# Optimization experiments

Hardware: AMD Instinct MI355X
Metric: run time of the kernel (lower is better)

## Reference

```python
import jax, jax.numpy as jnp
import numpy as np
from jax import lax

B, C, HID, H, W = 8, 256, 64, 64, 64

def conv3x3(x, w, b):
    # x: [B,C_in,H,W], w: [C_out,C_in,3,3], b: [C_out]
    y = lax.conv_general_dilated(x, w, window_strides=(1, 1), padding='SAME',
                                 dimension_numbers=('NCHW', 'OIHW', 'NCHW'))
    return y + b[None, :, None, None]

def setup_inputs() -> dict:
    key = jax.random.key(0)
    ks = jax.random.split(key, 7)
    s_in = 1.0 / np.sqrt(C * 9)
    return {
        'x': jax.random.normal(ks[0], (B, C, H, W), dtype=jnp.float32),
        'Wq': jax.random.normal(ks[1], (HID, C, 3, 3), dtype=jnp.float32) * s_in,
        'bq': jax.random.normal(ks[2], (HID,), dtype=jnp.float32) * s_in,
        'Wk': jax.random.normal(ks[3], (HID, C, 3, 3), dtype=jnp.float32) * s_in,
        'bk': jax.random.normal(ks[4], (HID,), dtype=jnp.float32) * s_in,
        'Wv': jax.random.normal(ks[5], (C, C, 3, 3), dtype=jnp.float32) * s_in,
        'bv': jax.random.normal(ks[6], (C,), dtype=jnp.float32) * s_in,
    }

def reference(x, Wq, bq, Wk, bk, Wv, bv):
    b, c, w, h = x.shape
    n = w * h
    q = conv3x3(x, Wq, bq).reshape(b, -1, n).transpose(0, 2, 1)  # [B,N,hid]
    k = conv3x3(x, Wk, bk).reshape(b, -1, n)                      # [B,hid,N]
    v = conv3x3(x, Wv, bv).reshape(b, c, n)                       # [B,C,N]
    attn = jax.nn.softmax(jnp.einsum('bnd,bdm->bnm', q, k), axis=-1)  # [B,N,N]
    # out = bmm(value, attn^T): out[b,c,m] = sum_n v[b,c,n] * attn[b,m,n]
    out = jnp.einsum('bcn,bmn->bcm', v, attn).reshape(b, c, w, h)
    # F.interpolate(out, h, mode='bilinear') with H==W is an exact identity
    return out + x
```

## Files before the change

### kernel.cpp

```cpp
#include <hip/hip_runtime.h>
#include <math.h>

#define NB   8
#define NC   256
#define ND   64
#define NPIX 4096

typedef short bf16x8 __attribute__((ext_vector_type(8)));
typedef float f32x4  __attribute__((ext_vector_type(4)));
typedef float f32x16 __attribute__((ext_vector_type(16)));

static __device__ __forceinline__ ushort f2bf(float f) {
    uint u = __float_as_uint(f);
    u += 0x7fffu + ((u >> 16) & 1u);
    return (ushort)(u >> 16);
}
static __device__ __forceinline__ float bf2f(ushort h) {
    return __uint_as_float(((uint)h) << 16);
}

__global__ __launch_bounds__(256) void prep_k(
    const float* __restrict__ x,
    const float* __restrict__ Wq, const float* __restrict__ Wk,
    const float* __restrict__ Wv,
    ushort* __restrict__ xth, ushort* __restrict__ xtl,
    ushort* __restrict__ qh, ushort* __restrict__ ql,
    ushort* __restrict__ kh, ushort* __restrict__ kl,
    ushort* __restrict__ vh)
{
    __shared__ char shbuf[64 * 68 * 4];
    const int id = blockIdx.x;
    const int t = threadIdx.x;

    if (id < 384) {
        float* wb = (float*)shbuf;
        const int g = id;
        const float* src;
        ushort *dh, *dl;
        int co, Co, split;
        if (g < 64)       { src = Wq + (size_t)g * 2304; co = g;       Co = 64;  dh = qh; dl = ql; split = 1; }
        else if (g < 128) { src = Wk + (size_t)(g - 64) * 2304; co = g - 64; Co = 64; dh = kh; dl = kl; split = 1; }
        else              { src = Wv + (size_t)(g - 128) * 2304; co = g - 128; Co = 256; dh = vh; dl = nullptr; split = 0; }

        for (int i = t; i < 2304; i += 256) wb[i] = src[i];
        __syncthreads();
        for (int j = t; j < 2304; j += 256) {
            const int rs = j >> 8, ci = j & 255;
            const float v = wb[ci * 9 + rs];
            const ushort hv = f2bf(v);
            const size_t o = ((size_t)((rs * 16 + (ci >> 4)) * Co + co)) * 16 + (ci & 15);
            dh[o] = hv;
            if (split) dl[o] = f2bf(v - bf2f(hv));
        }
    } else {
        float (*tile)[68] = (float(*)[68])shbuf;
        const int xid = id - 384;
        const int b = xid & 7;
        const int p0 = ((xid >> 3) & 63) * 64;
        const int c0 = (xid >> 9) * 64;

        const int cl = t >> 4, p4 = (t & 15) * 4;
        #pragma unroll
        for (int i = 0; i < 4; i++) {
            const int c = cl + 16 * i;
            *(float4*)&tile[c][p4] =
                *(const float4*)&x[((size_t)(b * NC + c0 + c)) * NPIX + p0 + p4];
        }
        __syncthreads();

        const int pl = t & 63, ch = t >> 6;
        float v[16];
        #pragma unroll
        for (int j = 0; j < 16; j++) v[j] = tile[ch * 16 + j][pl];
        ushort h[16], l[16];
        #pragma unroll
        for (int j = 0; j < 16; j++) {
            h[j] = f2bf(v[j]);
            l[j] = f2bf(v[j] - bf2f(h[j]));
        }
        const size_t o = ((size_t)(b * NPIX + p0 + pl)) * 256 + c0 + ch * 16;
        *(uint4*)&xth[o]     = *(uint4*)&h[0];
        *(uint4*)&xth[o + 8] = *(uint4*)&h[8];
        *(uint4*)&xtl[o]     = *(uint4*)&l[0];
        *(uint4*)&xtl[o + 8] = *(uint4*)&l[8];
    }
}

__global__ __launch_bounds__(256, 1) void conv_split_k(
    const ushort* __restrict__ xth, const ushort* __restrict__ xtl,
    const ushort* __restrict__ wqh, const ushort* __restrict__ wql,
    const ushort* __restrict__ wkh, const ushort* __restrict__ wkl,
    const float* __restrict__ bq, const float* __restrict__ bk,
    ushort* __restrict__ qoh, ushort* __restrict__ qol,
    ushort* __restrict__ koh, ushort* __restrict__ kol)
{
    extern __shared__ char smem[];
    ushort* xsh = (ushort*)smem;
    ushort* xsl = xsh + 6 * 66 * 24;
    float*  sbias = (float*)(xsl + 6 * 66 * 24);

    const int id = blockIdx.x;
    const int b = id & 7, hq = (id >> 3) & 15, ct = id >> 7;
    const ushort* wth = ct ? wkh : wqh;
    const ushort* wtl = ct ? wkl : wql;
    const float*  bias = ct ? bk : bq;
    ushort* outh = ct ? koh : qoh;
    ushort* outl = ct ? kol : qol;

    const int t = threadIdx.x;
    const int wv = t >> 6, lane = t & 63;
    const int l31 = lane & 31, khl = lane >> 5;
    const int lanebase = l31 * 24 + khl * 8;
    const int h = hq * 4 + wv;

    if (t < 64) sbias[t] = bias[t];
    for (int i = t; i < 384; i += 256) {
        const int p = i / 192, r2 = i % 192;
        const int row = r2 / 32, e = (r2 % 32) / 16, ci = r2 & 15;
        (p ? xsl : xsh)[(row * 66 + e * 65) * 24 + ci] = 0;
    }

    const int wlane = l31 * 16 + khl * 8;

    f32x16 a00 = {0}, a01 = {0}, a10 = {0}, a11 = {0};

    for (int ch = 0; ch < 16; ch++) {
        const int ci0 = ch * 16;

        bf16x8 whA0[9], whA1[9], wlA0[9], wlA1[9];
        #pragma unroll
        for (int rs = 0; rs < 9; rs++) {
            const size_t o = (size_t)(rs * 16 + ch) * 1024 + wlane;
            whA0[rs] = *(const bf16x8*)&wth[o];
            whA1[rs] = *(const bf16x8*)&wth[o + 512];
            wlA0[rs] = *(const bf16x8*)&wtl[o];
            wlA1[rs] = *(const bf16x8*)&wtl[o + 512];
        }

        __syncthreads();
        #pragma unroll
        for (int pl2 = 0; pl2 < 2; pl2++) {
            const ushort* src = pl2 ? xtl : xth;
            ushort* dst = pl2 ? xsl : xsh;
            #pragma unroll
            for (int i = 0; i < 3; i++) {
                const int a = i * 256 + t;
                const int cih = a & 1, col = (a >> 1) & 63, row = a >> 7;
                const int hs = hq * 4 + row - 1;
                uint4 val = {0, 0, 0, 0};
                if (hs >= 0 && hs < 64)
                    val = *(const uint4*)&src[((size_t)(b * NPIX + hs * 64 + col)) * 256 + ci0 + cih * 8];
                *(uint4*)&dst[(row * 66 + 1 + col) * 24 + cih * 8] = val;
            }
        }
        __syncthreads();

        #pragma unroll
        for (int rs = 0; rs < 9; rs++) {
            const int r = rs / 3, s = rs % 3;
            const int xo = ((wv + r) * 66 + s) * 24 + lanebase;
            bf16x8 B0h = *(const bf16x8*)&xsh[xo];
            bf16x8 B1h = *(const bf16x8*)&xsh[xo + 768];
            bf16x8 B0l = *(const bf16x8*)&xsl[xo];
            bf16x8 B1l = *(const bf16x8*)&xsl[xo + 768];
            a00 = __builtin_amdgcn_mfma_f32_32x32x16_bf16(whA0[rs], B0h, a00, 0, 0, 0);
            a01 = __builtin_amdgcn_mfma_f32_32x32x16_bf16(whA0[rs], B1h, a01, 0, 0, 0);
            a10 = __builtin_amdgcn_mfma_f32_32x32x16_bf16(whA1[rs], B0h, a10, 0, 0, 0);
            a11 = __builtin_amdgcn_mfma_f32_32x32x16_bf16(whA1[rs], B1h, a11, 0, 0, 0);
            a00 = __builtin_amdgcn_mfma_f32_32x32x16_bf16(whA0[rs], B0l, a00, 0, 0, 0);
            a01 = __builtin_amdgcn_mfma_f32_32x32x16_bf16(whA0[rs], B1l, a01, 0, 0, 0);
            a10 = __builtin_amdgcn_mfma_f32_32x32x16_bf16(whA1[rs], B0l, a10, 0, 0, 0);
            a11 = __builtin_amdgcn_mfma_f32_32x32x16_bf16(whA1[rs], B1l, a11, 0, 0, 0);
        }
        #pragma unroll
        for (int rs = 0; rs < 9; rs++) {
            const int r = rs / 3, s = rs % 3;
            const int xo = ((wv + r) * 66 + s) * 24 + lanebase;
            bf16x8 B0h = *(const bf16x8*)&xsh[xo];
            bf16x8 B1h = *(const bf16x8*)&xsh[xo + 768];
            a00 = __builtin_amdgcn_mfma_f32_32x32x16_bf16(wlA0[rs], B0h, a00, 0, 0, 0);
            a01 = __builtin_amdgcn_mfma_f32_32x32x16_bf16(wlA0[rs], B1h, a01, 0, 0, 0);
            a10 = __builtin_amdgcn_mfma_f32_32x32x16_bf16(wlA1[rs], B0h, a10, 0, 0, 0);
            a11 = __builtin_amdgcn_mfma_f32_32x32x16_bf16(wlA1[rs], B1h, a11, 0, 0, 0);
        }
    }

    const float4* sb4 = (const float4*)sbias;
    #pragma unroll
    for (int ms = 0; ms < 2; ms++)
        #pragma unroll
        for (int ns = 0; ns < 2; ns++) {
            const f32x16 av = ms ? (ns ? a11 : a10) : (ns ? a01 : a00);
            const int p = h * 64 + ns * 32 + l31;
            #pragma unroll
            for (int g = 0; g < 4; g++) {
                const float4 bi = sb4[ms * 8 + 2 * g + khl];
                float v0 = av[4 * g + 0] + bi.x;
                float v1 = av[4 * g + 1] + bi.y;
                float v2 = av[4 * g + 2] + bi.z;
                float v3 = av[4 * g + 3] + bi.w;
                ushort4 hv, lv;
                hv.x = f2bf(v0); lv.x = f2bf(v0 - bf2f(hv.x));
                hv.y = f2bf(v1); lv.y = f2bf(v1 - bf2f(hv.y));
                hv.z = f2bf(v2); lv.z = f2bf(v2 - bf2f(hv.z));
                hv.w = f2bf(v3); lv.w = f2bf(v3 - bf2f(hv.w));
                const size_t o = ((size_t)(b * NPIX + p)) * 64 + ms * 32 + 8 * g + 4 * khl;
                *(ushort4*)&outh[o] = hv;
                *(ushort4*)&outl[o] = lv;
            }
        }
}

__global__ __launch_bounds__(256, 2) void conv_v_k(
    const ushort* __restrict__ xth, const ushort* __restrict__ wtv,
    const float* __restrict__ bv, ushort* __restrict__ vout)
{
    extern __shared__ char smem[];
    ushort* xsh = (ushort*)smem;
    float*  sbias = (float*)(xsh + 6 * 66 * 24);

    const int id = blockIdx.x;
    const int b = id & 7, hq = (id >> 3) & 15, co0 = (id >> 7) * 64;
    const int t = threadIdx.x;
    const int wv = t >> 6, lane = t & 63;
    const int l31 = lane & 31, khl = lane >> 5;
    const int lanebase = l31 * 24 + khl * 8;
    const int h = hq * 4 + wv;

    if (t < 64) sbias[t] = bv[co0 + t];
    for (int i = t; i < 192; i += 256) {
        const int row = i / 32, e = (i % 32) / 16, ci = i & 15;
        xsh[(row * 66 + e * 65) * 24 + ci] = 0;
    }

    const int wlane = (co0 + l31) * 16 + khl * 8;

    f32x16 a00 = {0}, a01 = {0}, a10 = {0}, a11 = {0};

    for (int ch = 0; ch < 16; ch++) {
        const int ci0 = ch * 16;

        bf16x8 wB0[9], wB1[9];
        #pragma unroll
        for (int rs = 0; rs < 9; rs++) {
            const size_t o = (size_t)(rs * 16 + ch) * 4096 + wlane;
            wB0[rs] = *(const bf16x8*)&wtv[o];
            wB1[rs] = *(const bf16x8*)&wtv[o + 512];
        }

        __syncthreads();
        #pragma unroll
        for (int i = 0; i < 3; i++) {
            const int a = i * 256 + t;
            const int cih = a & 1, col = (a >> 1) & 63, row = a >> 7;
            const int hs = hq * 4 + row - 1;
            uint4 val = {0, 0, 0, 0};
            if (hs >= 0 && hs < 64)
                val = *(const uint4*)&xth[((size_t)(b * NPIX + hs * 64 + col)) * 256 + ci0 + cih * 8];
            *(uint4*)&xsh[(row * 66 + 1 + col) * 24 + cih * 8] = val;
        }
        __syncthreads();

        #pragma unroll
        for (int rs = 0; rs < 9; rs++) {
            const int r = rs / 3, s = rs % 3;
            const int xo = ((wv + r) * 66 + s) * 24 + lanebase;
            bf16x8 A0 = *(const bf16x8*)&xsh[xo];
            bf16x8 A1 = *(const bf16x8*)&xsh[xo + 768];
            a00 = __builtin_amdgcn_mfma_f32_32x32x16_bf16(A0, wB0[rs], a00, 0, 0, 0);
            a01 = __builtin_amdgcn_mfma_f32_32x32x16_bf16(A0, wB1[rs], a01, 0, 0, 0);
            a10 = __builtin_amdgcn_mfma_f32_32x32x16_bf16(A1, wB0[rs], a10, 0, 0, 0);
            a11 = __builtin_amdgcn_mfma_f32_32x32x16_bf16(A1, wB1[rs], a11, 0, 0, 0);
        }
    }

    #pragma unroll
    for (int ns = 0; ns < 2; ns++) {
        const int co = co0 + ns * 32 + l31;
        const float bi = sbias[ns * 32 + l31];
        #pragma unroll
        for (int ms = 0; ms < 2; ms++) {
            const f32x16 av = ms ? (ns ? a11 : a10) : (ns ? a01 : a00);
            #pragma unroll
            for (int g = 0; g < 4; g++) {
                const int p = h * 64 + ms * 32 + 8 * g + 4 * khl;
                ushort4 ov;
                ov.x = f2bf(av[4 * g + 0] + bi);
                ov.y = f2bf(av[4 * g + 1] + bi);
                ov.z = f2bf(av[4 * g + 2] + bi);
                ov.w = f2bf(av[4 * g + 3] + bi);
                *(ushort4*)&vout[((size_t)(b * NC + co)) * NPIX + p] = ov;
            }
        }
    }
}

__global__ __launch_bounds__(256, 2) void attn_k(
    const ushort* __restrict__ qh, const ushort* __restrict__ ql,
    const ushort* __restrict__ kh, const ushort* __restrict__ kl,
    const ushort* __restrict__ vb, const float* __restrict__ x,
    float* __restrict__ out)
{
    const int id = blockIdx.x;
    const int b  = id & 7;
    const int m0 = (id >> 3) * 64;
    const int t  = threadIdx.x;
    const int w  = t >> 6;
    const int lane = t & 63;
    const int quad = lane >> 4;
    const int l16  = lane & 15;

    __shared__ ushort sps[2][64 * 64];
    __shared__ float  red[4][64];
    __shared__ float  ivl[64];

    bf16x8 aqh[4][2], aql[4][2];
    #pragma unroll
    for (int mg = 0; mg < 4; mg++)
        #pragma unroll
        for (int ks = 0; ks < 2; ks++) {
            const size_t g = ((size_t)b * NPIX + m0 + mg * 16 + l16) * ND + ks * 32 + quad * 8;
            aqh[mg][ks] = *(const bf16x8*)&qh[g];
            aql[mg][ks] = *(const bf16x8*)&ql[g];
        }

    const size_t kbase = ((size_t)b * NPIX + 16 * w + l16) * ND + quad * 8;
    size_t vbase[4];
    #pragma unroll
    for (int ct = 0; ct < 4; ct++)
        vbase[ct] = ((size_t)b * NC + 64 * w + ct * 16 + l16) * NPIX + quad * 8;

    bf16x8 kfh[2], kfl[2], vf[4][2];
    #pragma unroll
    for (int ks = 0; ks < 2; ks++) {
        kfh[ks] = *(const bf16x8*)&kh[kbase + ks * 32];
        kfl[ks] = *(const bf16x8*)&kl[kbase + ks * 32];
    }
    #pragma unroll
    for (int ct = 0; ct < 4; ct++)
        #pragma unroll
        for (int ks = 0; ks < 2; ks++)
            vf[ct][ks] = *(const bf16x8*)&vb[vbase[ct] + ks * 32];

    f32x4 acc[4][4];
    #pragma unroll
    for (int i = 0; i < 4; i++)
        #pragma unroll
        for (int j = 0; j < 4; j++) acc[i][j] = (f32x4){0.f, 0.f, 0.f, 0.f};
    float lsum[4] = {0.f, 0.f, 0.f, 0.f};

    auto qk_tile = [&](int obuf) {
        #pragma unroll
        for (int mg = 0; mg < 4; mg++) {
            f32x4 s = {0.f, 0.f, 0.f, 0.f};
            #pragma unroll
            for (int ks = 0; ks < 2; ks++) {
                s = __builtin_amdgcn_mfma_f32_16x16x32_bf16(kfh[ks], aqh[mg][ks], s, 0, 0, 0);
                s = __builtin_amdgcn_mfma_f32_16x16x32_bf16(kfl[ks], aqh[mg][ks], s, 0, 0, 0);
                s = __builtin_amdgcn_mfma_f32_16x16x32_bf16(kfh[ks], aql[mg][ks], s, 0, 0, 0);
            }
            const ushort p0 = f2bf(__expf(s[0] - 30.f));
            const ushort p1 = f2bf(__expf(s[1] - 30.f));
            const ushort p2 = f2bf(__expf(s[2] - 30.f));
            const ushort p3 = f2bf(__expf(s[3] - 30.f));
            lsum[mg] += (bf2f(p0) + bf2f(p1)) + (bf2f(p2) + bf2f(p3));
            uint2 pk;
            pk.x = (uint)p0 | ((uint)p1 << 16);
            pk.y = (uint)p2 | ((uint)p3 << 16);
            const int row = mg * 16 + l16;
            const int bo = (32 * w + quad * 8) ^ ((row & 7) << 4);
            *(uint2*)((char*)&sps[obuf][0] + row * 128 + bo) = pk;
        }
    };

    qk_tile(0);
    {
        const size_t kb = kbase + (size_t)64 * ND;
        #pragma unroll
        for (int ks = 0; ks < 2; ks++) {
            kfh[ks] = *(const bf16x8*)&kh[kb + ks * 32];
            kfl[ks] = *(const bf16x8*)&kl[kb + ks * 32];
        }
    }
    asm volatile("s_waitcnt lgkmcnt(0)\n\ts_barrier" ::: "memory");

    for (int n0 = 0; n0 < NPIX; n0 += 64) {
        const int buf = (n0 >> 6) & 1;
        const bool nxt = (n0 + 64) < NPIX;

        bf16x8 ap[2][4];
        #pragma unroll
        for (int ks = 0; ks < 2; ks++)
            #pragma unroll
            for (int mg = 0; mg < 4; mg++) {
                const int row = mg * 16 + l16;
                const int bo = (ks * 64 + quad * 16) ^ ((row & 7) << 4);
                ap[ks][mg] = *(const bf16x8*)((const char*)&sps[buf][0] + row * 128 + bo);
            }

        if (nxt) qk_tile(buf ^ 1);

        #pragma unroll
        for (int ks = 0; ks < 2; ks++)
            #pragma unroll
            for (int mg = 0; mg < 4; mg++)
                #pragma unroll
                for (int ct = 0; ct < 4; ct++)
                    acc[mg][ct] = __builtin_amdgcn_mfma_f32_16x16x32_bf16(
                        ap[ks][mg], vf[ct][ks], acc[mg][ct], 0, 0, 0);

        if (n0 + 128 < NPIX) {
            const size_t kb = kbase + (size_t)(n0 + 128) * ND;
            #pragma unroll
            for (int ks = 0; ks < 2; ks++) {
                kfh[ks] = *(const bf16x8*)&kh[kb + ks * 32];
                kfl[ks] = *(const bf16x8*)&kl[kb + ks * 32];
            }
        }
        if (nxt) {
            #pragma unroll
            for (int ct = 0; ct < 4; ct++)
                #pragma unroll
                for (int ks = 0; ks < 2; ks++)
                    vf[ct][ks] = *(const bf16x8*)&vb[vbase[ct] + n0 + 64 + ks * 32];
        }

        asm volatile("s_waitcnt lgkmcnt(0)\n\ts_barrier" ::: "memory");
    }

    #pragma unroll
    for (int mg = 0; mg < 4; mg++) {
        lsum[mg] += __shfl_xor(lsum[mg], 16, 64);
        lsum[mg] += __shfl_xor(lsum[mg], 32, 64);
    }
    if (quad == 0) {
        #pragma unroll
        for (int mg = 0; mg < 4; mg++) red[w][mg * 16 + l16] = lsum[mg];
    }
    __syncthreads();
    if (t < 64)
        ivl[t] = 1.f / (red[0][t] + red[1][t] + red[2][t] + red[3][t]);
    __syncthreads();

    #pragma unroll
    for (int mg = 0; mg < 4; mg++) {
        const int mrow = mg * 16 + quad * 4;
        const float4 il4 = *(const float4*)&ivl[mrow];
        const int m = m0 + mrow;
        #pragma unroll
        for (int ct = 0; ct < 4; ct++) {
            const int c = 64 * w + ct * 16 + l16;
            const size_t base = ((size_t)b * NC + c) * NPIX + m;
            const float4 xv = *(const float4*)&x[base];
            const f32x4 a = acc[mg][ct];
            float4 o;
            o.x = fmaf(a[0], il4.x, xv.x);
            o.y = fmaf(a[1], il4.y, xv.y);
            o.z = fmaf(a[2], il4.z, xv.z);
            o.w = fmaf(a[3], il4.w, xv.w);
            *(float4*)&out[base] = o;
        }
    }
}

extern "C" void kernel_launch(void* const* d_in, const int* in_sizes, int n_in,
                              void* d_out, int out_size, void* d_ws, size_t ws_size,
                              hipStream_t stream)
{
    const float* x  = (const float*)d_in[0];
    const float* Wq = (const float*)d_in[1];
    const float* bq = (const float*)d_in[2];
    const float* Wk = (const float*)d_in[3];
    const float* bk = (const float*)d_in[4];
    const float* Wv = (const float*)d_in[5];
    const float* bv = (const float*)d_in[6];
    float* outp = (float*)d_out;

    const size_t XT = (size_t)NB * NPIX * 256;
    const size_t QK = (size_t)NB * NPIX * ND;
    ushort* xt_h = (ushort*)d_ws;
    ushort* xt_l = xt_h + XT;
    ushort* v_b  = xt_l;
    ushort* q_h  = xt_l + XT;
    ushort* q_l  = q_h + QK;
    ushort* k_h  = q_l + QK;
    ushort* k_l  = k_h + QK;
    ushort* wtq_h = k_l + QK;
    ushort* wtq_l = wtq_h + 147456;
    ushort* wtk_h = wtq_l + 147456;
    ushort* wtk_l = wtk_h + 147456;
    ushort* wtv_h = wtk_l + 147456;

    dim3 blk(256);
    prep_k<<<dim3(2432), blk, 0, stream>>>(
        x, Wq, Wk, Wv, xt_h, xt_l, wtq_h, wtq_l, wtk_h, wtk_l, wtv_h);
    conv_split_k<<<dim3(256), blk, 38272, stream>>>(
        xt_h, xt_l, wtq_h, wtq_l, wtk_h, wtk_l, bq, bk, q_h, q_l, k_h, k_l);
    conv_v_k<<<dim3(512), blk, 19264, stream>>>(xt_h, wtv_h, bv, v_b);
    attn_k<<<dim3(512), blk, 0, stream>>>(q_h, q_l, k_h, k_l, v_b, x, outp);
}
```

Baseline: 406.2 us.

## Double-buffer LDS input tiles and prefetch weights in conv kernels

Both 3x3 conv kernels now keep two LDS halo-tile buffers. Each iteration issues the global loads for the next channel chunk into registers before the MFMA loop and writes them into the alternate buffer afterwards, which cuts the per-chunk barriers from two to one. Weight fragments for the next chunk are also reloaded between MFMA phases instead of at the top of the loop. The aim is to hide global memory latency behind compute, at the cost of doubled LDS use and extra registers.

```diff
diff --git a/kernel.cpp b/kernel.cpp
--- a/kernel.cpp
+++ b/kernel.cpp
@@ -95,9 +95,8 @@
     ushort* __restrict__ koh, ushort* __restrict__ kol)
 {
     extern __shared__ char smem[];
-    ushort* xsh = (ushort*)smem;
-    ushort* xsl = xsh + 6 * 66 * 24;
-    float*  sbias = (float*)(xsl + 6 * 66 * 24);
+    ushort* xbase = (ushort*)smem;
+    float*  sbias = (float*)(xbase + 38016);
 
     const int id = blockIdx.x;
     const int b = id & 7, hq = (id >> 3) & 15, ct = id >> 7;
@@ -114,46 +113,72 @@
     const int h = hq * 4 + wv;
 
     if (t < 64) sbias[t] = bias[t];
-    for (int i = t; i < 384; i += 256) {
-        const int p = i / 192, r2 = i % 192;
+    for (int i = t; i < 768; i += 256) {
+        const int pl = i / 192, r2 = i % 192;
         const int row = r2 / 32, e = (r2 % 32) / 16, ci = r2 & 15;
-        (p ? xsl : xsh)[(row * 66 + e * 65) * 24 + ci] = 0;
-    }
-
+        xbase[pl * 9504 + (row * 66 + e * 65) * 24 + ci] = 0;
+    }
+
+    int xrow[3], xcol[3], xcih[3];
+    bool xval[3];
+    #pragma unroll
+    for (int i = 0; i < 3; i++) {
+        const int a = i * 256 + t;
+        xcih[i] = a & 1; xcol[i] = (a >> 1) & 63; xrow[i] = a >> 7;
+        const int hs = hq * 4 + xrow[i] - 1;
+        xval[i] = (hs >= 0 && hs < 64);
+    }
     const int wlane = l31 * 16 + khl * 8;
 
     f32x16 a00 = {0}, a01 = {0}, a10 = {0}, a11 = {0};
 
-    for (int ch = 0; ch < 16; ch++) {
-        const int ci0 = ch * 16;
-
-        bf16x8 whA0[9], whA1[9], wlA0[9], wlA1[9];
+    bf16x8 whA0[9], whA1[9], wlA0[9], wlA1[9];
+
+    {
+        #pragma unroll
+        for (int i = 0; i < 3; i++) {
+            const int hs = hq * 4 + xrow[i] - 1;
+            uint4 vh4 = {0,0,0,0}, vl4 = {0,0,0,0};
+            if (xval[i]) {
+                const size_t g = ((size_t)(b * NPIX + hs * 64 + xcol[i])) * 256 + xcih[i] * 8;
+                vh4 = *(const uint4*)&xth[g];
+                vl4 = *(const uint4*)&xtl[g];
+            }
+            const int o = (xrow[i] * 66 + 1 + xcol[i]) * 24 + xcih[i] * 8;
+            *(uint4*)&xbase[o]        = vh4;
+            *(uint4*)&xbase[9504 + o] = vl4;
+        }
         #pragma unroll
         for (int rs = 0; rs < 9; rs++) {
-            const size_t o = (size_t)(rs * 16 + ch) * 1024 + wlane;
+            const size_t o = (size_t)(rs * 16) * 1024 + wlane;
             whA0[rs] = *(const bf16x8*)&wth[o];
             whA1[rs] = *(const bf16x8*)&wth[o + 512];
             wlA0[rs] = *(const bf16x8*)&wtl[o];
             wlA1[rs] = *(const bf16x8*)&wtl[o + 512];
         }
-
-        __syncthreads();
-        #pragma unroll
-        for (int pl2 = 0; pl2 < 2; pl2++) {
-            const ushort* src = pl2 ? xtl : xth;
-            ushort* dst = pl2 ? xsl : xsh;
+    }
+    asm volatile("s_waitcnt lgkmcnt(0)\n\ts_barrier" ::: "memory");
+
+    for (int ch = 0; ch < 16; ch++) {
+        const int cur = ch & 1;
+        ushort* xsh = xbase + cur * 19008;
+        ushort* xsl = xsh + 9504;
+        const bool nxt = ch < 15;
+        const int ci0n = (ch + 1) * 16;
+
+        uint4 xrh[3], xrl[3];
+        if (nxt) {
             #pragma unroll
             for (int i = 0; i < 3; i++) {
-                const int a = i * 256 + t;
-                const int cih = a & 1, col = (a >> 1) & 63, row = a >> 7;
-                const int hs = hq * 4 + row - 1;
-                uint4 val = {0, 0, 0, 0};
-                if (hs >= 0 && hs < 64)
-                    val = *(const uint4*)&src[((size_t)(b * NPIX + hs * 64 + col)) * 256 + ci0 + cih * 8];
-                *(uint4*)&dst[(row * 66 + 1 + col) * 24 + cih * 8] = val;
-            }
-        }
-        __syncthreads();
+                const int hs = hq * 4 + xrow[i] - 1;
+                xrh[i] = (uint4){0,0,0,0}; xrl[i] = (uint4){0,0,0,0};
+                if (xval[i]) {
+                    const size_t g = ((size_t)(b * NPIX + hs * 64 + xcol[i])) * 256 + ci0n + xcih[i] * 8;
+                    xrh[i] = *(const uint4*)&xth[g];
+                    xrl[i] = *(const uint4*)&xtl[g];
+                }
+            }
+        }
 
         #pragma unroll
         for (int rs = 0; rs < 9; rs++) {
@@ -172,6 +197,14 @@
             a10 = __builtin_amdgcn_mfma_f32_32x32x16_bf16(whA1[rs], B0l, a10, 0, 0, 0);
             a11 = __builtin_amdgcn_mfma_f32_32x32x16_bf16(whA1[rs], B1l, a11, 0, 0, 0);
         }
+        if (nxt) {
+            #pragma unroll
+            for (int rs = 0; rs < 9; rs++) {
+                const size_t o = (size_t)(rs * 16 + ch + 1) * 1024 + wlane;
+                whA0[rs] = *(const bf16x8*)&wth[o];
+                whA1[rs] = *(const bf16x8*)&wth[o + 512];
+            }
+        }
         #pragma unroll
         for (int rs = 0; rs < 9; rs++) {
             const int r = rs / 3, s = rs % 3;
@@ -182,6 +215,23 @@
             a01 = __builtin_amdgcn_mfma_f32_32x32x16_bf16(wlA0[rs], B1h, a01, 0, 0, 0);
             a10 = __builtin_amdgcn_mfma_f32_32x32x16_bf16(wlA1[rs], B0h, a10, 0, 0, 0);
             a11 = __builtin_amdgcn_mfma_f32_32x32x16_bf16(wlA1[rs], B1h, a11, 0, 0, 0);
+        }
+        if (nxt) {
+            #pragma unroll
+            for (int rs = 0; rs < 9; rs++) {
+                const size_t o = (size_t)(rs * 16 + ch + 1) * 1024 + wlane;
+                wlA0[rs] = *(const bf16x8*)&wtl[o];
+                wlA1[rs] = *(const bf16x8*)&wtl[o + 512];
+            }
+            ushort* dsh = xbase + (cur ^ 1) * 19008;
+            ushort* dsl = dsh + 9504;
+            #pragma unroll
+            for (int i = 0; i < 3; i++) {
+                const int o = (xrow[i] * 66 + 1 + xcol[i]) * 24 + xcih[i] * 8;
+                *(uint4*)&dsh[o] = xrh[i];
+                *(uint4*)&dsl[o] = xrl[i];
+            }
+            asm volatile("s_waitcnt lgkmcnt(0)\n\ts_barrier" ::: "memory");
         }
     }
 
@@ -216,8 +266,8 @@
     const float* __restrict__ bv, ushort* __restrict__ vout)
 {
     extern __shared__ char smem[];
-    ushort* xsh = (ushort*)smem;
-    float*  sbias = (float*)(xsh + 6 * 66 * 24);
+    ushort* xbase = (ushort*)smem;
+    float*  sbias = (float*)(xbase + 19008);
 
     const int id = blockIdx.x;
     const int b = id & 7, hq = (id >> 3) & 15, co0 = (id >> 7) * 64;
@@ -228,38 +278,61 @@
     const int h = hq * 4 + wv;
 
     if (t < 64) sbias[t] = bv[co0 + t];
-    for (int i = t; i < 192; i += 256) {
-        const int row = i / 32, e = (i % 32) / 16, ci = i & 15;
-        xsh[(row * 66 + e * 65) * 24 + ci] = 0;
-    }
-
+    for (int i = t; i < 384; i += 256) {
+        const int pl = i / 192, r2 = i % 192;
+        const int row = r2 / 32, e = (r2 % 32) / 16, ci = r2 & 15;
+        xbase[pl * 9504 + (row * 66 + e * 65) * 24 + ci] = 0;
+    }
+
+    int xrow[3], xcol[3], xcih[3];
+    bool xval[3];
+    #pragma unroll
+    for (int i = 0; i < 3; i++) {
+        const int a = i * 256 + t;
+        xcih[i] = a & 1; xcol[i] = (a >> 1) & 63; xrow[i] = a >> 7;
+        const int hs = hq * 4 + xrow[i] - 1;
+        xval[i] = (hs >= 0 && hs < 64);
+    }
     const int wlane = (co0 + l31) * 16 + khl * 8;
 
     f32x16 a00 = {0}, a01 = {0}, a10 = {0}, a11 = {0};
 
-    for (int ch = 0; ch < 16; ch++) {
-        const int ci0 = ch * 16;
-
-        bf16x8 wB0[9], wB1[9];
+    bf16x8 wB0[9], wB1[9];
+
+    {
+        #pragma unroll
+        for (int i = 0; i < 3; i++) {
+            const int hs = hq * 4 + xrow[i] - 1;
+            uint4 v4 = {0,0,0,0};
+            if (xval[i])
+                v4 = *(const uint4*)&xth[((size_t)(b * NPIX + hs * 64 + xcol[i])) * 256 + xcih[i] * 8];
+            *(uint4*)&xbase[(xrow[i] * 66 + 1 + xcol[i]) * 24 + xcih[i] * 8] = v4;
+        }
         #pragma unroll
         for (int rs = 0; rs < 9; rs++) {
-            const size_t o = (size_t)(rs * 16 + ch) * 4096 + wlane;
+            const size_t o = (size_t)(rs * 16) * 4096 + wlane;
             wB0[rs] = *(const bf16x8*)&wtv[o];
             wB1[rs] = *(const bf16x8*)&wtv[o + 512];
         }
-
-        __syncthreads();
-        #pragma unroll
-        for (int i = 0; i < 3; i++) {
-            const int a = i * 256 + t;
-            const int cih = a & 1, col = (a >> 1) & 63, row = a >> 7;
-            const int hs = hq * 4 + row - 1;
-            uint4 val = {0, 0, 0, 0};
-            if (hs >= 0 && hs < 64)
-                val = *(const uint4*)&xth[((size_t)(b * NPIX + hs * 64 + col)) * 256 + ci0 + cih * 8];
-            *(uint4*)&xsh[(row * 66 + 1 + col) * 24 + cih * 8] = val;
-        }
-        __syncthreads();
+    }
+    asm volatile("s_waitcnt lgkmcnt(0)\n\ts_barrier" ::: "memory");
+
+    for (int ch = 0; ch < 16; ch++) {
+        const int cur = ch & 1;
+        ushort* xsh = xbase + cur * 9504;
+        const bool nxt = ch < 15;
+        const int ci0n = (ch + 1) * 16;
+
+        uint4 xr[3];
+        if (nxt) {
+            #pragma unroll
+            for (int i = 0; i < 3; i++) {
+                const int hs = hq * 4 + xrow[i] - 1;
+                xr[i] = (uint4){0,0,0,0};
+                if (xval[i])
+                    xr[i] = *(const uint4*)&xth[((size_t)(b * NPIX + hs * 64 + xcol[i])) * 256 + ci0n + xcih[i] * 8];
+            }
+        }
 
         #pragma unroll
         for (int rs = 0; rs < 9; rs++) {
@@ -271,6 +344,20 @@
             a01 = __builtin_amdgcn_mfma_f32_32x32x16_bf16(A0, wB1[rs], a01, 0, 0, 0);
             a10 = __builtin_amdgcn_mfma_f32_32x32x16_bf16(A1, wB0[rs], a10, 0, 0, 0);
             a11 = __builtin_amdgcn_mfma_f32_32x32x16_bf16(A1, wB1[rs], a11, 0, 0, 0);
+        }
+
+        if (nxt) {
+            #pragma unroll
+            for (int rs = 0; rs < 9; rs++) {
+                const size_t o = (size_t)(rs * 16 + ch + 1) * 4096 + wlane;
+                wB0[rs] = *(const bf16x8*)&wtv[o];
+                wB1[rs] = *(const bf16x8*)&wtv[o + 512];
+            }
+            ushort* dsh = xbase + (cur ^ 1) * 9504;
+            #pragma unroll
+            for (int i = 0; i < 3; i++)
+                *(uint4*)&dsh[(xrow[i] * 66 + 1 + xcol[i]) * 24 + xcih[i] * 8] = xr[i];
+            asm volatile("s_waitcnt lgkmcnt(0)\n\ts_barrier" ::: "memory");
         }
     }
 
@@ -494,8 +581,8 @@
     dim3 blk(256);
     prep_k<<<dim3(2432), blk, 0, stream>>>(
         x, Wq, Wk, Wv, xt_h, xt_l, wtq_h, wtq_l, wtk_h, wtk_l, wtv_h);
-    conv_split_k<<<dim3(256), blk, 38272, stream>>>(
+    conv_split_k<<<dim3(256), blk, 76288, stream>>>(
         xt_h, xt_l, wtq_h, wtq_l, wtk_h, wtk_l, bq, bk, q_h, q_l, k_h, k_l);
-    conv_v_k<<<dim3(512), blk, 19264, stream>>>(xt_h, wtv_h, bv, v_b);
+    conv_v_k<<<dim3(512), blk, 38272, stream>>>(xt_h, wtv_h, bv, v_b);
     attn_k<<<dim3(512), blk, 0, stream>>>(q_h, q_l, k_h, k_l, v_b, x, outp);
 }
```

After: 382.9 us. -5.7%, faster.
